# Optimization experiments

Measured on AMD Instinct MI355X. Metric: run time of the kernel, lower is better.

## Reference

```python
import jax, jax.numpy as jnp
import numpy as np

SIGMA = 0.15
POS_W, ANG_W, WID_W, SCORE_W = 1.0, 1.0, 1.0, 0.5


def setup_inputs() -> dict:
    N, MAXC = 262144, 32
    rng = np.random.default_rng(0)
    counts = rng.integers(0, MAXC, size=N)
    M = int(counts.sum())
    key = jax.random.key(0)
    k1, k2, k3 = jax.random.split(key, 3)
    pred = jax.random.normal(k1, (N, 6), jnp.float32)
    gt = jax.random.normal(k2, (M, 6), jnp.float32)
    # GT score is a BCE target: keep it in [0, 1)
    gt = gt.at[:, 5].set(jax.random.uniform(k3, (M,), jnp.float32))
    return {
        "pred": pred,
        "all_gt_grasps": gt,
        "gt_counts": jnp.asarray(counts, jnp.int32),
    }


def reference(pred, all_gt_grasps, gt_counts):
    N = pred.shape[0]
    M = all_gt_grasps.shape[0]
    # CSR-style ragged layout: segment id of each GT row
    seg = jnp.repeat(jnp.arange(N), gt_counts, total_repeat_length=M)  # (M,)
    has_gt = gt_counts > 0                                             # (N,)

    # Step 1: squared distance from each GT to its prediction's center
    ppos = pred[seg, :2]                                               # (M,2)
    sq_dist = jnp.sum((ppos - all_gt_grasps[:, :2]) ** 2, axis=1)      # (M,)

    # Step 2: Gaussian tolerance position loss (per-segment max response)
    resp = jnp.exp(-sq_dist / (2.0 * SIGMA ** 2))
    max_resp = jax.ops.segment_max(resp, seg, num_segments=N)
    loss_pos = jnp.where(has_gt, 1.0 - max_resp, 0.0)

    # Step 3: nearest GT per prediction (first argmin, matching torch.argmin)
    seg_min = jax.ops.segment_min(sq_dist, seg, num_segments=N)
    cand = jnp.where(sq_dist == seg_min[seg], jnp.arange(M), M)
    nearest = jax.ops.segment_min(cand, seg, num_segments=N)
    nearest = jnp.where(has_gt, jnp.minimum(nearest, M - 1), 0)
    ng = all_gt_grasps[nearest]                                        # (N,6)

    # Step 4: angle (L1 on cos/sin), width (smooth L1), score (BCE-with-logits)
    loss_angle = jnp.where(
        has_gt,
        jnp.abs(pred[:, 2] - ng[:, 2]) + jnp.abs(pred[:, 3] - ng[:, 3]),
        0.0,
    )
    d = pred[:, 4] - ng[:, 4]
    ad = jnp.abs(d)
    smooth_l1 = jnp.where(ad < 1.0, 0.5 * d * d, ad - 0.5)
    loss_width = jnp.where(has_gt, smooth_l1, 0.0)

    x, t = pred[:, 5], ng[:, 5]
    bce = jnp.maximum(x, 0.0) - x * t + jnp.log1p(jnp.exp(-jnp.abs(x)))
    loss_score = jnp.where(has_gt & (t > 0), bce, 0.0)

    lp = loss_pos.mean()
    la = loss_angle.mean()
    lw = loss_width.mean()
    ls = loss_score.mean()
    lg = POS_W * lp + ANG_W * la + WID_W * lw + SCORE_W * ls
    return jnp.stack([lp, la, lw, ls, lg])
```

## Files before the change

kernel.cpp:

```cpp
#include <hip/hip_runtime.h>
#include <math.h>
#include <float.h>

#define BS 256
#define MAXC 31
#define MAXGT (BS * MAXC)
typedef unsigned long long u64;
typedef unsigned char u8;


__global__ void block_sum_kernel(const int* __restrict__ counts,
                                 int* __restrict__ blockSums, int N) {
    int i = blockIdx.x * BS + threadIdx.x;
    int v = (i < N) ? counts[i] : 0;
    for (int o = 32; o > 0; o >>= 1) v += __shfl_down(v, o, 64);
    __shared__ int ws[BS / 64];
    int lane = threadIdx.x & 63, w = threadIdx.x >> 6;
    if (lane == 0) ws[w] = v;
    __syncthreads();
    if (threadIdx.x == 0) {
        int s = 0;
        for (int ww = 0; ww < BS / 64; ++ww) s += ws[ww];
        blockSums[blockIdx.x] = s;
    }
}

__global__ void scan_kernel(const int* __restrict__ blockSums,
                            int* __restrict__ blockOffsets, int nb) {
    __shared__ int tmp[1024];
    int t = threadIdx.x;
    int v = (t < nb) ? blockSums[t] : 0;
    tmp[t] = v;
    __syncthreads();
    for (int off = 1; off < 1024; off <<= 1) {
        int x = (t >= off) ? tmp[t - off] : 0;
        __syncthreads();
        tmp[t] += x;
        __syncthreads();
    }
    if (t < nb) blockOffsets[t] = tmp[t] - v;
}

__global__ void __launch_bounds__(BS)
fused_kernel(const float* __restrict__ pred, const float* __restrict__ gt,
             const int* __restrict__ counts, const int* __restrict__ blockOffsets,
             float4* __restrict__ partials, int N) {
    const int t = threadIdx.x;
    const int b = blockIdx.x;
    const int i = b * BS + t;
    const int lane = t & 63, w = t >> 6;

    __shared__ u8 ownerMap[MAXGT];
    __shared__ float2 pxy[BS];
    __shared__ u64 bestLds[BS];
    __shared__ int waveTot[BS / 64];
    __shared__ int sTotal;
    __shared__ float red[BS / 64][4];

    const int c = (i < N) ? counts[i] : 0;
    int incl = c;
    for (int o = 1; o < 64; o <<= 1) {
        int x = __shfl_up(incl, o, 64);
        if (lane >= o) incl += x;
    }
    if (lane == 63) waveTot[w] = incl;
    __syncthreads();
    int wbase = 0;
    for (int ww = 0; ww < w; ++ww) wbase += waveTot[ww];
    const int localStart = wbase + incl - c;
    if (t == BS - 1) sTotal = localStart + c;
    bestLds[t] = ~0ULL;
    if (i < N) pxy[t] = reinterpret_cast<const float2*>(pred)[(size_t)i * 3];
    for (int j = 0; j < c; ++j) ownerMap[localStart + j] = (u8)t;
    __syncthreads();

    const int base = blockOffsets[b];
    const int blockTotal = sTotal;
    const float2* gxy = reinterpret_cast<const float2*>(gt);

    for (int tile = 0; tile < blockTotal; tile += BS * 4) {
        int j[4]; float2 g[4]; bool valid[4];
#pragma unroll
        for (int u = 0; u < 4; ++u) {
            j[u] = tile + u * BS + t;
            valid[u] = j[u] < blockTotal;
            if (valid[u]) g[u] = gxy[(size_t)(base + j[u]) * 3];
        }
#pragma unroll
        for (int u = 0; u < 4; ++u) {
            if (valid[u]) {
                const int owner = (int)ownerMap[j[u]];
                const float2 p = pxy[owner];
                const float dx = p.x - g[u].x, dy = p.y - g[u].y;
                const float d2 = dx * dx + dy * dy;
                const u64 key = ((u64)__float_as_uint(d2) << 32)
                              | (unsigned int)(base + j[u]);
                if (key < bestLds[owner]) atomicMin(&bestLds[owner], key);
            }
        }
    }
    __syncthreads();

    float lp = 0.f, la = 0.f, lw = 0.f, ls = 0.f;
    if (i < N && c > 0) {
        const u64 key = bestLds[t];
        const float d2 = __uint_as_float((unsigned int)(key >> 32));
        const int bj = (int)(key & 0xffffffffu);
        lp = 1.0f - expf(-d2 / 0.045f);

        const float* p = pred + (size_t)i * 6;
        const float2 p23 = *reinterpret_cast<const float2*>(p + 2);
        const float2 p45 = *reinterpret_cast<const float2*>(p + 4);
        const float* ng = gt + (size_t)bj * 6;
        const float2 g23 = *reinterpret_cast<const float2*>(ng + 2);
        const float2 g45 = *reinterpret_cast<const float2*>(ng + 4);

        la = fabsf(p23.x - g23.x) + fabsf(p23.y - g23.y);
        const float d = p45.x - g45.x;
        const float ad = fabsf(d);
        lw = (ad < 1.0f) ? 0.5f * d * d : ad - 0.5f;
        const float x = p45.y;
        if (g45.y > 0.0f) {
            ls = fmaxf(x, 0.0f) - x * g45.y + log1pf(expf(-fabsf(x)));
        }
    }

    for (int o = 32; o > 0; o >>= 1) {
        lp += __shfl_down(lp, o, 64);
        la += __shfl_down(la, o, 64);
        lw += __shfl_down(lw, o, 64);
        ls += __shfl_down(ls, o, 64);
    }
    if (lane == 0) { red[w][0] = lp; red[w][1] = la; red[w][2] = lw; red[w][3] = ls; }
    __syncthreads();
    if (t == 0) {
        float s0 = 0, s1 = 0, s2 = 0, s3 = 0;
        for (int ww = 0; ww < BS / 64; ++ww) {
            s0 += red[ww][0]; s1 += red[ww][1]; s2 += red[ww][2]; s3 += red[ww][3];
        }
        partials[b] = make_float4(s0, s1, s2, s3);
    }
}

__global__ void finalize_kernel(const float4* __restrict__ partials,
                                float* __restrict__ out, int nb, int N) {
    const int t = threadIdx.x;
    const int lane = t & 63, w = t >> 6;
    double s0 = 0, s1 = 0, s2 = 0, s3 = 0;
    if (t < nb) {
        const float4 v = partials[t];
        s0 = v.x; s1 = v.y; s2 = v.z; s3 = v.w;
    }
    for (int o = 32; o > 0; o >>= 1) {
        s0 += __shfl_down(s0, o, 64);
        s1 += __shfl_down(s1, o, 64);
        s2 += __shfl_down(s2, o, 64);
        s3 += __shfl_down(s3, o, 64);
    }
    __shared__ double red[16][4];
    if (lane == 0) { red[w][0] = s0; red[w][1] = s1; red[w][2] = s2; red[w][3] = s3; }
    __syncthreads();
    if (t == 0) {
        double t0 = 0, t1 = 0, t2 = 0, t3 = 0;
        for (int ww = 0; ww < blockDim.x / 64; ++ww) {
            t0 += red[ww][0]; t1 += red[ww][1]; t2 += red[ww][2]; t3 += red[ww][3];
        }
        const double inv = 1.0 / (double)N;
        const float lp = (float)(t0 * inv);
        const float la = (float)(t1 * inv);
        const float lw = (float)(t2 * inv);
        const float ls = (float)(t3 * inv);
        out[0] = lp; out[1] = la; out[2] = lw; out[3] = ls;
        out[4] = lp + la + lw + 0.5f * ls;
    }
}

extern "C" void kernel_launch(void* const* d_in, const int* in_sizes, int n_in,
                              void* d_out, int out_size, void* d_ws, size_t ws_size,
                              hipStream_t stream) {
    const float* pred = (const float*)d_in[0];
    const float* gt = (const float*)d_in[1];
    const int* counts = (const int*)d_in[2];
    float* out = (float*)d_out;

    const int N = in_sizes[2];
    const int numBlocks = (N + BS - 1) / BS;

    int* blockSums = (int*)d_ws;
    int* blockOffsets = (int*)((char*)d_ws + 4096);
    float4* partials = (float4*)((char*)d_ws + 8192);

    block_sum_kernel<<<numBlocks, BS, 0, stream>>>(counts, blockSums, N);
    scan_kernel<<<1, 1024, 0, stream>>>(blockSums, blockOffsets, numBlocks);
    fused_kernel<<<numBlocks, BS, 0, stream>>>(pred, gt, counts, blockOffsets,
                                               partials, N);
    finalize_kernel<<<1, 1024, 0, stream>>>(partials, out, numBlocks, N);
}
```

Measured before the change: 165.8 us.

## Coalesce GT loads through shared-memory tile and use wave-shuffle block scan

The GT xy loads used a 24-byte stride per thread. They are replaced by fully coalesced float2 loads of whole GT rows into a shared tile, from which each thread then reads its xy. The block-offset scan drops the 10-step shared-memory Hillis-Steele loop for a two-level wave-shuffle scan with fewer barriers. In exchange the main loop now needs two syncthreads per 256-row tile instead of none, unrolling drops from 4 to 1 (less memory-level parallelism), and the kernel uses an extra 6KB of LDS.

Result: no change. 165.8 us (+0.0%).

```diff
diff --git a/kernel.cpp b/kernel.cpp
--- a/kernel.cpp
+++ b/kernel.cpp
@@ -27,18 +27,27 @@
 
 __global__ void scan_kernel(const int* __restrict__ blockSums,
                             int* __restrict__ blockOffsets, int nb) {
-    __shared__ int tmp[1024];
-    int t = threadIdx.x;
-    int v = (t < nb) ? blockSums[t] : 0;
-    tmp[t] = v;
-    __syncthreads();
-    for (int off = 1; off < 1024; off <<= 1) {
-        int x = (t >= off) ? tmp[t - off] : 0;
-        __syncthreads();
-        tmp[t] += x;
-        __syncthreads();
-    }
-    if (t < nb) blockOffsets[t] = tmp[t] - v;
+    const int t = threadIdx.x, lane = t & 63, w = t >> 6;
+    __shared__ int wt[16];
+    const int v = (t < nb) ? blockSums[t] : 0;
+    int incl = v;
+    for (int o = 1; o < 64; o <<= 1) {
+        int x = __shfl_up(incl, o, 64);
+        if (lane >= o) incl += x;
+    }
+    if (lane == 63) wt[w] = incl;
+    __syncthreads();
+    if (w == 0 && lane < 16) {
+        const int x = wt[lane];
+        int wi = x;
+        for (int o = 1; o < 16; o <<= 1) {
+            int y = __shfl_up(wi, o, 64);
+            if (lane >= o) wi += y;
+        }
+        wt[lane] = wi - x;
+    }
+    __syncthreads();
+    if (t < nb) blockOffsets[t] = wt[w] + incl - v;
 }
 
 __global__ void __launch_bounds__(BS)
@@ -51,6 +60,7 @@
     const int lane = t & 63, w = t >> 6;
 
     __shared__ u8 ownerMap[MAXGT];
+    __shared__ float2 tile[BS * 3];
     __shared__ float2 pxy[BS];
     __shared__ u64 bestLds[BS];
     __shared__ int waveTot[BS / 64];
@@ -76,30 +86,34 @@
 
     const int base = blockOffsets[b];
     const int blockTotal = sTotal;
-    const float2* gxy = reinterpret_cast<const float2*>(gt);
-
-    for (int tile = 0; tile < blockTotal; tile += BS * 4) {
-        int j[4]; float2 g[4]; bool valid[4];
-#pragma unroll
-        for (int u = 0; u < 4; ++u) {
-            j[u] = tile + u * BS + t;
-            valid[u] = j[u] < blockTotal;
-            if (valid[u]) g[u] = gxy[(size_t)(base + j[u]) * 3];
-        }
-#pragma unroll
-        for (int u = 0; u < 4; ++u) {
-            if (valid[u]) {
-                const int owner = (int)ownerMap[j[u]];
-                const float2 p = pxy[owner];
-                const float dx = p.x - g[u].x, dy = p.y - g[u].y;
-                const float d2 = dx * dx + dy * dy;
-                const u64 key = ((u64)__float_as_uint(d2) << 32)
-                              | (unsigned int)(base + j[u]);
-                if (key < bestLds[owner]) atomicMin(&bestLds[owner], key);
-            }
-        }
-    }
-    __syncthreads();
+    const int total2 = blockTotal * 3;
+    const float2* g2 = reinterpret_cast<const float2*>(gt) + (size_t)base * 3;
+
+    for (int tileRow = 0; tileRow < blockTotal; tileRow += BS) {
+        const int e0 = tileRow * 3;
+        float2 r0, r1, r2;
+        const int i0 = e0 + t, i1 = e0 + t + BS, i2 = e0 + t + 2 * BS;
+        if (i0 < total2) r0 = g2[i0];
+        if (i1 < total2) r1 = g2[i1];
+        if (i2 < total2) r2 = g2[i2];
+        if (i0 < total2) tile[t] = r0;
+        if (i1 < total2) tile[t + BS] = r1;
+        if (i2 < total2) tile[t + 2 * BS] = r2;
+        __syncthreads();
+
+        const int j = tileRow + t;
+        if (j < blockTotal) {
+            const float2 g = tile[t * 3];
+            const int owner = (int)ownerMap[j];
+            const float2 p = pxy[owner];
+            const float dx = p.x - g.x, dy = p.y - g.y;
+            const float d2 = dx * dx + dy * dy;
+            const u64 key = ((u64)__float_as_uint(d2) << 32)
+                          | (unsigned int)(base + j);
+            if (key < bestLds[owner]) atomicMin(&bestLds[owner], key);
+        }
+        __syncthreads();
+    }
 
     float lp = 0.f, la = 0.f, lw = 0.f, ls = 0.f;
     if (i < N && c > 0) {
```

## Merge block-sum into single-block scan and fold finalize into last-block reduction

Applied to the files above, without the earlier changes.

The per-block count sums are now computed inside the single 1024-thread scan kernel, which reads all counts itself, and the separate finalize kernel is replaced by a last-block-done pattern with an atomic counter inside the fused kernel. This cuts the pipeline from four launches to two, removing launch gaps and inter-kernel dependencies. In exchange, one workgroup now reads all 1 MB of counts serially, and every block pays atomic exchanges, a fence and a counter increment at the end.

Result: slower. 238.3 us (+43.7%).

```diff
diff --git a/kernel.cpp b/kernel.cpp
--- a/kernel.cpp
+++ b/kernel.cpp
@@ -9,42 +9,51 @@
 typedef unsigned char u8;
 
 
-__global__ void block_sum_kernel(const int* __restrict__ counts,
-                                 int* __restrict__ blockSums, int N) {
-    int i = blockIdx.x * BS + threadIdx.x;
-    int v = (i < N) ? counts[i] : 0;
-    for (int o = 32; o > 0; o >>= 1) v += __shfl_down(v, o, 64);
-    __shared__ int ws[BS / 64];
-    int lane = threadIdx.x & 63, w = threadIdx.x >> 6;
-    if (lane == 0) ws[w] = v;
-    __syncthreads();
-    if (threadIdx.x == 0) {
+__global__ void __launch_bounds__(1024)
+scan_kernel(const int* __restrict__ counts, int* __restrict__ blockOffsets,
+            int* __restrict__ done, int N, int nb) {
+    __shared__ int cs[1024];
+    __shared__ int wt[16];
+    const int t = threadIdx.x, lane = t & 63, w = t >> 6;
+    for (int k = 0; k < 64; ++k) {
+        const int c = w * 64 + k;
         int s = 0;
-        for (int ww = 0; ww < BS / 64; ++ww) s += ws[ww];
-        blockSums[blockIdx.x] = s;
-    }
-}
-
-__global__ void scan_kernel(const int* __restrict__ blockSums,
-                            int* __restrict__ blockOffsets, int nb) {
-    __shared__ int tmp[1024];
-    int t = threadIdx.x;
-    int v = (t < nb) ? blockSums[t] : 0;
-    tmp[t] = v;
-    __syncthreads();
-    for (int off = 1; off < 1024; off <<= 1) {
-        int x = (t >= off) ? tmp[t - off] : 0;
-        __syncthreads();
-        tmp[t] += x;
-        __syncthreads();
-    }
-    if (t < nb) blockOffsets[t] = tmp[t] - v;
+#pragma unroll
+        for (int q = 0; q < 4; ++q) {
+            const int idx = c * BS + q * 64 + lane;
+            s += (idx < N) ? counts[idx] : 0;
+        }
+        for (int o = 32; o > 0; o >>= 1) s += __shfl_down(s, o, 64);
+        if (lane == 0) cs[c] = s;
+    }
+    if (t == 0) *done = 0;
+    __syncthreads();
+    const int v = (t < nb) ? cs[t] : 0;
+    int incl = v;
+    for (int o = 1; o < 64; o <<= 1) {
+        int x = __shfl_up(incl, o, 64);
+        if (lane >= o) incl += x;
+    }
+    if (lane == 63) wt[w] = incl;
+    __syncthreads();
+    if (w == 0 && lane < 16) {
+        const int x = wt[lane];
+        int wi = x;
+        for (int o = 1; o < 16; o <<= 1) {
+            int y = __shfl_up(wi, o, 64);
+            if (lane >= o) wi += y;
+        }
+        wt[lane] = wi - x;
+    }
+    __syncthreads();
+    if (t < nb) blockOffsets[t] = wt[w] + incl - v;
 }
 
 __global__ void __launch_bounds__(BS)
 fused_kernel(const float* __restrict__ pred, const float* __restrict__ gt,
              const int* __restrict__ counts, const int* __restrict__ blockOffsets,
-             float4* __restrict__ partials, int N) {
+             float* __restrict__ partials, int* __restrict__ done,
+             float* __restrict__ out, int N, int nb) {
     const int t = threadIdx.x;
     const int b = blockIdx.x;
     const int i = b * BS + t;
@@ -56,6 +65,7 @@
     __shared__ int waveTot[BS / 64];
     __shared__ int sTotal;
     __shared__ float red[BS / 64][4];
+    __shared__ int lastFlag;
 
     const int c = (i < N) ? counts[i] : 0;
     int incl = c;
@@ -138,40 +148,46 @@
         for (int ww = 0; ww < BS / 64; ++ww) {
             s0 += red[ww][0]; s1 += red[ww][1]; s2 += red[ww][2]; s3 += red[ww][3];
         }
-        partials[b] = make_float4(s0, s1, s2, s3);
-    }
-}
-
-__global__ void finalize_kernel(const float4* __restrict__ partials,
-                                float* __restrict__ out, int nb, int N) {
-    const int t = threadIdx.x;
-    const int lane = t & 63, w = t >> 6;
-    double s0 = 0, s1 = 0, s2 = 0, s3 = 0;
-    if (t < nb) {
-        const float4 v = partials[t];
-        s0 = v.x; s1 = v.y; s2 = v.z; s3 = v.w;
-    }
-    for (int o = 32; o > 0; o >>= 1) {
-        s0 += __shfl_down(s0, o, 64);
-        s1 += __shfl_down(s1, o, 64);
-        s2 += __shfl_down(s2, o, 64);
-        s3 += __shfl_down(s3, o, 64);
-    }
-    __shared__ double red[16][4];
-    if (lane == 0) { red[w][0] = s0; red[w][1] = s1; red[w][2] = s2; red[w][3] = s3; }
-    __syncthreads();
-    if (t == 0) {
-        double t0 = 0, t1 = 0, t2 = 0, t3 = 0;
-        for (int ww = 0; ww < blockDim.x / 64; ++ww) {
-            t0 += red[ww][0]; t1 += red[ww][1]; t2 += red[ww][2]; t3 += red[ww][3];
-        }
-        const double inv = 1.0 / (double)N;
-        const float lp = (float)(t0 * inv);
-        const float la = (float)(t1 * inv);
-        const float lw = (float)(t2 * inv);
-        const float ls = (float)(t3 * inv);
-        out[0] = lp; out[1] = la; out[2] = lw; out[3] = ls;
-        out[4] = lp + la + lw + 0.5f * ls;
+        atomicExch(&partials[b * 4 + 0], s0);
+        atomicExch(&partials[b * 4 + 1], s1);
+        atomicExch(&partials[b * 4 + 2], s2);
+        atomicExch(&partials[b * 4 + 3], s3);
+        __threadfence();
+        const int prev = atomicAdd(done, 1);
+        lastFlag = (prev == nb - 1) ? 1 : 0;
+    }
+    __syncthreads();
+    if (lastFlag) {
+        __threadfence();
+        double s0 = 0, s1 = 0, s2 = 0, s3 = 0;
+        for (int q = t; q < nb; q += BS) {
+            s0 += (double)atomicAdd(&partials[q * 4 + 0], 0.0f);
+            s1 += (double)atomicAdd(&partials[q * 4 + 1], 0.0f);
+            s2 += (double)atomicAdd(&partials[q * 4 + 2], 0.0f);
+            s3 += (double)atomicAdd(&partials[q * 4 + 3], 0.0f);
+        }
+        for (int o = 32; o > 0; o >>= 1) {
+            s0 += __shfl_down(s0, o, 64);
+            s1 += __shfl_down(s1, o, 64);
+            s2 += __shfl_down(s2, o, 64);
+            s3 += __shfl_down(s3, o, 64);
+        }
+        __shared__ double dred[BS / 64][4];
+        if (lane == 0) { dred[w][0] = s0; dred[w][1] = s1; dred[w][2] = s2; dred[w][3] = s3; }
+        __syncthreads();
+        if (t == 0) {
+            double t0 = 0, t1 = 0, t2 = 0, t3 = 0;
+            for (int ww = 0; ww < BS / 64; ++ww) {
+                t0 += dred[ww][0]; t1 += dred[ww][1]; t2 += dred[ww][2]; t3 += dred[ww][3];
+            }
+            const double inv = 1.0 / (double)N;
+            const float flp = (float)(t0 * inv);
+            const float fla = (float)(t1 * inv);
+            const float flw = (float)(t2 * inv);
+            const float fls = (float)(t3 * inv);
+            out[0] = flp; out[1] = fla; out[2] = flw; out[3] = fls;
+            out[4] = flp + fla + flw + 0.5f * fls;
+        }
     }
 }
 
@@ -184,15 +200,13 @@
     float* out = (float*)d_out;
 
     const int N = in_sizes[2];
-    const int numBlocks = (N + BS - 1) / BS;
-
-    int* blockSums = (int*)d_ws;
-    int* blockOffsets = (int*)((char*)d_ws + 4096);
-    float4* partials = (float4*)((char*)d_ws + 8192);
-
-    block_sum_kernel<<<numBlocks, BS, 0, stream>>>(counts, blockSums, N);
-    scan_kernel<<<1, 1024, 0, stream>>>(blockSums, blockOffsets, numBlocks);
-    fused_kernel<<<numBlocks, BS, 0, stream>>>(pred, gt, counts, blockOffsets,
-                                               partials, N);
-    finalize_kernel<<<1, 1024, 0, stream>>>(partials, out, numBlocks, N);
+    const int nb = (N + BS - 1) / BS;
+
+    int* blockOffsets = (int*)d_ws;
+    int* done = (int*)((char*)d_ws + 4096);
+    float* partials = (float*)((char*)d_ws + 8192);
+
+    scan_kernel<<<1, 1024, 0, stream>>>(counts, blockOffsets, done, N, nb);
+    fused_kernel<<<nb, BS, 0, stream>>>(pred, gt, counts, blockOffsets,
+                                        partials, done, out, N, nb);
 }
```

## Halve rows per block, keep 256 threads, stage pred rows in LDS with float4 loads

Applied to the files above, without the earlier changes.

Each 256-thread block now owns 128 predictions instead of 256, which doubles the block count and gives each segment more threads for the GT sweep. The 8x-unrolled GT loop and float4 staging of whole pred rows in LDS aim to raise memory-level parallelism and to avoid strided global pred reads in the epilogue. The scan becomes a two-element-per-thread wavefront scan so it can handle up to 2048 blocks, and finalize uses a strided loop for the same reason. Half the threads sit idle in the prefix and epilogue phases, and the pred float4 load assumes N is a multiple of 128.

Result: slower. 172.1 us (+3.8%).

```diff
diff --git a/kernel.cpp b/kernel.cpp
--- a/kernel.cpp
+++ b/kernel.cpp
@@ -2,62 +2,74 @@
 #include <math.h>
 #include <float.h>
 
-#define BS 256
+#define ROWS 128
+#define TPB 256
 #define MAXC 31
-#define MAXGT (BS * MAXC)
+#define MAXGT (ROWS * MAXC)
 typedef unsigned long long u64;
 typedef unsigned char u8;
 
 
 __global__ void block_sum_kernel(const int* __restrict__ counts,
                                  int* __restrict__ blockSums, int N) {
-    int i = blockIdx.x * BS + threadIdx.x;
-    int v = (i < N) ? counts[i] : 0;
+    const int base = blockIdx.x * ROWS;
+    const int i0 = base + threadIdx.x, i1 = base + 64 + threadIdx.x;
+    int v = ((i0 < N) ? counts[i0] : 0) + ((i1 < N) ? counts[i1] : 0);
     for (int o = 32; o > 0; o >>= 1) v += __shfl_down(v, o, 64);
-    __shared__ int ws[BS / 64];
-    int lane = threadIdx.x & 63, w = threadIdx.x >> 6;
-    if (lane == 0) ws[w] = v;
-    __syncthreads();
-    if (threadIdx.x == 0) {
-        int s = 0;
-        for (int ww = 0; ww < BS / 64; ++ww) s += ws[ww];
-        blockSums[blockIdx.x] = s;
-    }
+    if (threadIdx.x == 0) blockSums[blockIdx.x] = v;
 }
 
 __global__ void scan_kernel(const int* __restrict__ blockSums,
                             int* __restrict__ blockOffsets, int nb) {
-    __shared__ int tmp[1024];
-    int t = threadIdx.x;
-    int v = (t < nb) ? blockSums[t] : 0;
-    tmp[t] = v;
-    __syncthreads();
-    for (int off = 1; off < 1024; off <<= 1) {
-        int x = (t >= off) ? tmp[t - off] : 0;
-        __syncthreads();
-        tmp[t] += x;
-        __syncthreads();
-    }
-    if (t < nb) blockOffsets[t] = tmp[t] - v;
-}
-
-__global__ void __launch_bounds__(BS)
+    const int t = threadIdx.x, lane = t & 63, w = t >> 6;
+    __shared__ int wt[16];
+    const int e0 = 2 * t, e1 = 2 * t + 1;
+    const int v0 = (e0 < nb) ? blockSums[e0] : 0;
+    const int v1 = (e1 < nb) ? blockSums[e1] : 0;
+    const int s = v0 + v1;
+    int incl = s;
+    for (int o = 1; o < 64; o <<= 1) {
+        int x = __shfl_up(incl, o, 64);
+        if (lane >= o) incl += x;
+    }
+    if (lane == 63) wt[w] = incl;
+    __syncthreads();
+    if (w == 0 && lane < 16) {
+        const int x = wt[lane];
+        int wi = x;
+        for (int o = 1; o < 16; o <<= 1) {
+            int y = __shfl_up(wi, o, 64);
+            if (lane >= o) wi += y;
+        }
+        wt[lane] = wi - x;
+    }
+    __syncthreads();
+    const int excl = wt[w] + incl - s;
+    if (e0 < nb) blockOffsets[e0] = excl;
+    if (e1 < nb) blockOffsets[e1] = excl + v0;
+}
+
+__global__ void __launch_bounds__(TPB)
 fused_kernel(const float* __restrict__ pred, const float* __restrict__ gt,
              const int* __restrict__ counts, const int* __restrict__ blockOffsets,
              float4* __restrict__ partials, int N) {
     const int t = threadIdx.x;
     const int b = blockIdx.x;
-    const int i = b * BS + t;
     const int lane = t & 63, w = t >> 6;
 
     __shared__ u8 ownerMap[MAXGT];
-    __shared__ float2 pxy[BS];
-    __shared__ u64 bestLds[BS];
-    __shared__ int waveTot[BS / 64];
+    __shared__ float predS[ROWS * 6];
+    __shared__ u64 bestLds[ROWS];
+    __shared__ int waveTot[TPB / 64];
     __shared__ int sTotal;
-    __shared__ float red[BS / 64][4];
-
-    const int c = (i < N) ? counts[i] : 0;
+    __shared__ float red[TPB / 64][4];
+
+    if (t < ROWS * 6 / 4) {
+        const float4 v = reinterpret_cast<const float4*>(pred)[(size_t)b * (ROWS * 6 / 4) + t];
+        reinterpret_cast<float4*>(predS)[t] = v;
+    }
+    const int i = b * ROWS + t;
+    const int c = (t < ROWS && i < N) ? counts[i] : 0;
     int incl = c;
     for (int o = 1; o < 64; o <<= 1) {
         int x = __shfl_up(incl, o, 64);
@@ -68,9 +80,8 @@
     int wbase = 0;
     for (int ww = 0; ww < w; ++ww) wbase += waveTot[ww];
     const int localStart = wbase + incl - c;
-    if (t == BS - 1) sTotal = localStart + c;
-    bestLds[t] = ~0ULL;
-    if (i < N) pxy[t] = reinterpret_cast<const float2*>(pred)[(size_t)i * 3];
+    if (t == ROWS - 1) sTotal = localStart + c;
+    if (t < ROWS) bestLds[t] = ~0ULL;
     for (int j = 0; j < c; ++j) ownerMap[localStart + j] = (u8)t;
     __syncthreads();
 
@@ -78,20 +89,20 @@
     const int blockTotal = sTotal;
     const float2* gxy = reinterpret_cast<const float2*>(gt);
 
-    for (int tile = 0; tile < blockTotal; tile += BS * 4) {
-        int j[4]; float2 g[4]; bool valid[4];
+    for (int tile = 0; tile < blockTotal; tile += TPB * 8) {
+        int j[8]; float2 g[8]; bool valid[8];
 #pragma unroll
-        for (int u = 0; u < 4; ++u) {
-            j[u] = tile + u * BS + t;
+        for (int u = 0; u < 8; ++u) {
+            j[u] = tile + u * TPB + t;
             valid[u] = j[u] < blockTotal;
             if (valid[u]) g[u] = gxy[(size_t)(base + j[u]) * 3];
         }
 #pragma unroll
-        for (int u = 0; u < 4; ++u) {
+        for (int u = 0; u < 8; ++u) {
             if (valid[u]) {
                 const int owner = (int)ownerMap[j[u]];
-                const float2 p = pxy[owner];
-                const float dx = p.x - g[u].x, dy = p.y - g[u].y;
+                const float px = predS[owner * 6], py = predS[owner * 6 + 1];
+                const float dx = px - g[u].x, dy = py - g[u].y;
                 const float d2 = dx * dx + dy * dy;
                 const u64 key = ((u64)__float_as_uint(d2) << 32)
                               | (unsigned int)(base + j[u]);
@@ -102,26 +113,24 @@
     __syncthreads();
 
     float lp = 0.f, la = 0.f, lw = 0.f, ls = 0.f;
-    if (i < N && c > 0) {
+    if (t < ROWS && i < N && c > 0) {
         const u64 key = bestLds[t];
         const float d2 = __uint_as_float((unsigned int)(key >> 32));
         const int bj = (int)(key & 0xffffffffu);
         lp = 1.0f - expf(-d2 / 0.045f);
 
-        const float* p = pred + (size_t)i * 6;
-        const float2 p23 = *reinterpret_cast<const float2*>(p + 2);
-        const float2 p45 = *reinterpret_cast<const float2*>(p + 4);
+        const float p2 = predS[t * 6 + 2], p3 = predS[t * 6 + 3];
+        const float p4 = predS[t * 6 + 4], p5 = predS[t * 6 + 5];
         const float* ng = gt + (size_t)bj * 6;
         const float2 g23 = *reinterpret_cast<const float2*>(ng + 2);
         const float2 g45 = *reinterpret_cast<const float2*>(ng + 4);
 
-        la = fabsf(p23.x - g23.x) + fabsf(p23.y - g23.y);
-        const float d = p45.x - g45.x;
+        la = fabsf(p2 - g23.x) + fabsf(p3 - g23.y);
+        const float d = p4 - g45.x;
         const float ad = fabsf(d);
         lw = (ad < 1.0f) ? 0.5f * d * d : ad - 0.5f;
-        const float x = p45.y;
         if (g45.y > 0.0f) {
-            ls = fmaxf(x, 0.0f) - x * g45.y + log1pf(expf(-fabsf(x)));
+            ls = fmaxf(p5, 0.0f) - p5 * g45.y + log1pf(expf(-fabsf(p5)));
         }
     }
 
@@ -135,7 +144,7 @@
     __syncthreads();
     if (t == 0) {
         float s0 = 0, s1 = 0, s2 = 0, s3 = 0;
-        for (int ww = 0; ww < BS / 64; ++ww) {
+        for (int ww = 0; ww < TPB / 64; ++ww) {
             s0 += red[ww][0]; s1 += red[ww][1]; s2 += red[ww][2]; s3 += red[ww][3];
         }
         partials[b] = make_float4(s0, s1, s2, s3);
@@ -147,9 +156,9 @@
     const int t = threadIdx.x;
     const int lane = t & 63, w = t >> 6;
     double s0 = 0, s1 = 0, s2 = 0, s3 = 0;
-    if (t < nb) {
-        const float4 v = partials[t];
-        s0 = v.x; s1 = v.y; s2 = v.z; s3 = v.w;
+    for (int q = t; q < nb; q += 1024) {
+        const float4 v = partials[q];
+        s0 += v.x; s1 += v.y; s2 += v.z; s3 += v.w;
     }
     for (int o = 32; o > 0; o >>= 1) {
         s0 += __shfl_down(s0, o, 64);
@@ -162,7 +171,7 @@
     __syncthreads();
     if (t == 0) {
         double t0 = 0, t1 = 0, t2 = 0, t3 = 0;
-        for (int ww = 0; ww < blockDim.x / 64; ++ww) {
+        for (int ww = 0; ww < 16; ++ww) {
             t0 += red[ww][0]; t1 += red[ww][1]; t2 += red[ww][2]; t3 += red[ww][3];
         }
         const double inv = 1.0 / (double)N;
@@ -184,15 +193,15 @@
     float* out = (float*)d_out;
 
     const int N = in_sizes[2];
-    const int numBlocks = (N + BS - 1) / BS;
+    const int nb = (N + ROWS - 1) / ROWS;
 
     int* blockSums = (int*)d_ws;
-    int* blockOffsets = (int*)((char*)d_ws + 4096);
-    float4* partials = (float4*)((char*)d_ws + 8192);
-
-    block_sum_kernel<<<numBlocks, BS, 0, stream>>>(counts, blockSums, N);
-    scan_kernel<<<1, 1024, 0, stream>>>(blockSums, blockOffsets, numBlocks);
-    fused_kernel<<<numBlocks, BS, 0, stream>>>(pred, gt, counts, blockOffsets,
-                                               partials, N);
-    finalize_kernel<<<1, 1024, 0, stream>>>(partials, out, numBlocks, N);
-}
+    int* blockOffsets = (int*)((char*)d_ws + 8192);
+    float4* partials = (float4*)((char*)d_ws + 16384);
+
+    block_sum_kernel<<<nb, 64, 0, stream>>>(counts, blockSums, N);
+    scan_kernel<<<1, 1024, 0, stream>>>(blockSums, blockOffsets, nb);
+    fused_kernel<<<nb, TPB, 0, stream>>>(pred, gt, counts, blockOffsets,
+                                         partials, N);
+    finalize_kernel<<<1, 1024, 0, stream>>>(partials, out, nb, N);
+}
```
